# Optimization experiments

Hardware: AMD Instinct MI355X
Metric: run time of the kernel (lower is better)

## Reference

```python
import jax, jax.numpy as jnp
import numpy as np
from jax import lax

KERNEL_SIZE = 5
BOUNDARY_WIDTH = 10


def setup_inputs() -> dict:
    key = jax.random.key(0)
    x_in = jax.random.normal(key, (4, 16, 720, 1440), dtype=jnp.float32)
    return {"x_in": x_in}


def _box_sum(a, k):
    """Sum over a k x k window on the last two dims, zero-padded (SAME).
    Zero padding + mask-count division reproduces the clipped-window average."""
    window = (1,) * (a.ndim - 2) + (k, k)
    strides = (1,) * a.ndim
    return lax.reduce_window(a, jnp.array(0, a.dtype), lax.add, window, strides, "SAME")


def reference(x_in) -> jnp.ndarray:
    k = KERNEL_SIZE
    bw = BOUNDARY_WIDTH
    H, W = x_in.shape[-2], x_in.shape[-1]

    ii = jnp.arange(H)
    jj = jnp.arange(W)
    # boundary mask [H, W]: True within boundary_width of any edge
    mb = (((ii < bw) | (ii >= H - bw))[:, None]
          | ((jj < bw) | (jj >= W - bw))[None, :])
    mb_f = mb.astype(x_in.dtype)
    mi_f = 1.0 - mb_f

    # windowed sums of same-class neighbors (zero padding = clipped window)
    num_b = _box_sum(x_in * mb_f, k)   # contributions from boundary pixels
    num_i = _box_sum(x_in * mi_f, k)   # contributions from interior pixels
    cnt_b = _box_sum(mb_f, k)          # [H, W] counts, broadcast over leading dims
    cnt_i = _box_sum(mi_f, k)

    num = jnp.where(mb, num_b, num_i)
    cnt = jnp.where(mb, cnt_b, cnt_i)  # >= 1 wherever selected (pixel counts itself)
    return num / cnt
```

## Files before the change

### kernel.cpp

```cpp
#include <hip/hip_runtime.h>


#define HH 720
#define WW 1440
#define PLANE (HH * WW)
#define NPLANES 64


#define NG 354
#define NCHUNK 29
#define CHUNK 24

__device__ __forceinline__ float4 hsum5(const float* __restrict__ p) {
    const float2 l = *(const float2*)(p - 2);
    const float4 m = *(const float4*)(p);
    const float2 r = *(const float2*)(p + 4);
    float4 h;
    h.x = l.x + l.y + m.x + m.y + m.z;
    h.y = h.x - l.x + m.w;
    h.z = h.y - l.y + r.x;
    h.w = h.z - m.x + r.y;
    return h;
}

__global__ __launch_bounds__(256) void fast_kernel(const float* __restrict__ x,
                                                   float* __restrict__ out) {
    const int id = blockIdx.x * 256 + threadIdx.x;
    if (id >= NG * NCHUNK) return;
    const int chunk = id / NG;
    const int g     = id - chunk * NG;
    const int j0    = 12 + 4 * g;
    const int row0  = 12 + chunk * CHUNK;

    const float* __restrict__ xp = x + (size_t)blockIdx.y * PLANE;
    float* __restrict__ op       = out + (size_t)blockIdx.y * PLANE;

    float4 h[5];
#pragma unroll
    for (int t = 0; t < 4; ++t) {
        h[t] = hsum5(xp + (row0 - 2 + t) * WW + j0);
    }

#pragma unroll
    for (int t = 0; t < CHUNK; ++t) {
        const int r = row0 + t;
        h[(t + 4) % 5] = hsum5(xp + (r + 2) * WW + j0);
        float4 v;
        v.x = ((h[0].x + h[1].x) + (h[2].x + h[3].x)) + h[4].x;
        v.y = ((h[0].y + h[1].y) + (h[2].y + h[3].y)) + h[4].y;
        v.z = ((h[0].z + h[1].z) + (h[2].z + h[3].z)) + h[4].z;
        v.w = ((h[0].w + h[1].w) + (h[2].w + h[3].w)) + h[4].w;
        const float s = 1.0f / 25.0f;
        v.x *= s; v.y *= s; v.z *= s; v.w *= s;
        *(float4*)(op + r * WW + j0) = v;
    }
}


#define NEDGE 51264

__global__ __launch_bounds__(256) void edge_kernel(const float* __restrict__ x,
                                                   float* __restrict__ out) {
    const int p = blockIdx.x * 256 + threadIdx.x;
    if (p >= NEDGE) return;
    int i, j;
    if (p < 34560) {
        i = p / 1440;
        j = p - i * 1440;
        if (i >= 12) i += 696;
    } else {
        const int q  = p - 34560;
        const int qi = q / 24;
        const int r  = q - qi * 24;
        i = 12 + qi;
        j = (r < 12) ? r : r + 1416;
    }

    const float* __restrict__ xp = x + (size_t)blockIdx.y * PLANE;
    const bool cb = (i < 10) | (i >= 710) | (j < 10) | (j >= 1430);

    float s = 0.0f, cnt = 0.0f;
#pragma unroll
    for (int di = -2; di <= 2; ++di) {
#pragma unroll
        for (int dj = -2; dj <= 2; ++dj) {
            const int ni = i + di, nj = j + dj;
            const bool inb = ((unsigned)ni < (unsigned)HH) & ((unsigned)nj < (unsigned)WW);
            const bool nb  = (ni < 10) | (ni >= 710) | (nj < 10) | (nj >= 1430);
            const int ci = min(max(ni, 0), HH - 1);
            const int cj = min(max(nj, 0), WW - 1);
            const float v = xp[ci * WW + cj];
            const float w = (inb && (nb == cb)) ? 1.0f : 0.0f;
            s += w * v;
            cnt += w;
        }
    }
    out[(size_t)blockIdx.y * PLANE + i * WW + j] = s / cnt;
}

extern "C" void kernel_launch(void* const* d_in, const int* in_sizes, int n_in,
                              void* d_out, int out_size, void* d_ws, size_t ws_size,
                              hipStream_t stream) {
    const float* x = (const float*)d_in[0];
    float* out = (float*)d_out;

    dim3 gf((NG * NCHUNK + 255) / 256, NPLANES);
    hipLaunchKernelGGL(fast_kernel, gf, dim3(256), 0, stream, x, out);

    dim3 ge((NEDGE + 255) / 256, NPLANES);
    hipLaunchKernelGGL(edge_kernel, ge, dim3(256), 0, stream, x, out);
}
```

Before: 469.2 us.

## Fuse interior and edge kernels; widen to 8 columns with running vertical sum

Merges the interior fast kernel and the edge kernel into one launch, dispatching on blockIdx.x. Each interior thread now covers 8 columns instead of 4 and keeps a running vertical sum (add new row, subtract old) instead of re-adding all five row sums. Output writes use nontemporal stores. This removes a kernel launch and some redundant horizontal loads and adds, but raises register pressure per thread and halves the number of interior threads.

```diff
diff --git a/kernel.cpp b/kernel.cpp
--- a/kernel.cpp
+++ b/kernel.cpp
@@ -6,62 +6,77 @@
 #define PLANE (HH * WW)
 #define NPLANES 64
 
-
-#define NG 354
+#define NG8 177
 #define NCHUNK 29
 #define CHUNK 24
+#define NFAST (NG8 * NCHUNK)
+#define FAST_BLOCKS 21
 
-__device__ __forceinline__ float4 hsum5(const float* __restrict__ p) {
+#define NEDGE 51264
+#define EDGE_BLOCKS 201
+
+typedef float v4f __attribute__((ext_vector_type(4)));
+
+__device__ __forceinline__ void hsum8(const float* __restrict__ p, float h[8]) {
     const float2 l = *(const float2*)(p - 2);
-    const float4 m = *(const float4*)(p);
-    const float2 r = *(const float2*)(p + 4);
-    float4 h;
-    h.x = l.x + l.y + m.x + m.y + m.z;
-    h.y = h.x - l.x + m.w;
-    h.z = h.y - l.y + r.x;
-    h.w = h.z - m.x + r.y;
-    return h;
+    const float4 a = *(const float4*)(p);
+    const float4 b = *(const float4*)(p + 4);
+    const float2 r = *(const float2*)(p + 8);
+    h[0] = l.x + l.y + a.x + a.y + a.z;
+    h[1] = h[0] - l.x + a.w;
+    h[2] = h[1] - l.y + b.x;
+    h[3] = h[2] - a.x + b.y;
+    h[4] = h[3] - a.y + b.z;
+    h[5] = h[4] - a.z + b.w;
+    h[6] = h[5] - a.w + r.x;
+    h[7] = h[6] - b.x + r.y;
 }
 
-__global__ __launch_bounds__(256) void fast_kernel(const float* __restrict__ x,
-                                                   float* __restrict__ out) {
-    const int id = blockIdx.x * 256 + threadIdx.x;
-    if (id >= NG * NCHUNK) return;
-    const int chunk = id / NG;
-    const int g     = id - chunk * NG;
-    const int j0    = 12 + 4 * g;
-    const int row0  = 12 + chunk * CHUNK;
-
+__global__ __launch_bounds__(256) void smooth_kernel(const float* __restrict__ x,
+                                                     float* __restrict__ out) {
     const float* __restrict__ xp = x + (size_t)blockIdx.y * PLANE;
     float* __restrict__ op       = out + (size_t)blockIdx.y * PLANE;
 
-    float4 h[5];
+    if (blockIdx.x < FAST_BLOCKS) {
+        const int id = blockIdx.x * 256 + threadIdx.x;
+        if (id >= NFAST) return;
+        const int chunk = id / NG8;
+        const int g     = id - chunk * NG8;
+        const int j0    = 12 + 8 * g;
+        const int row0  = 12 + chunk * CHUNK;
+
+        float h[5][8];
+        float V[8];
+
 #pragma unroll
-    for (int t = 0; t < 4; ++t) {
-        h[t] = hsum5(xp + (row0 - 2 + t) * WW + j0);
+        for (int t = 0; t < 4; ++t) {
+            hsum8(xp + (row0 - 2 + t) * WW + j0, h[t]);
+        }
+#pragma unroll
+        for (int c = 0; c < 8; ++c) V[c] = h[0][c] + h[1][c] + h[2][c] + h[3][c];
+
+#pragma unroll
+        for (int t = 0; t < CHUNK; ++t) {
+            const int r = row0 + t;
+            float* hn = h[(t + 4) % 5];
+            const float* ho = h[t % 5];
+            hsum8(xp + (r + 2) * WW + j0, hn);
+
+            const float s = 1.0f / 25.0f;
+#pragma unroll
+            for (int c = 0; c < 8; ++c) V[c] += hn[c];
+            v4f v0, v1;
+            v0.x = V[0] * s; v0.y = V[1] * s; v0.z = V[2] * s; v0.w = V[3] * s;
+            v1.x = V[4] * s; v1.y = V[5] * s; v1.z = V[6] * s; v1.w = V[7] * s;
+            __builtin_nontemporal_store(v0, (v4f*)(op + r * WW + j0));
+            __builtin_nontemporal_store(v1, (v4f*)(op + r * WW + j0 + 4));
+#pragma unroll
+            for (int c = 0; c < 8; ++c) V[c] -= ho[c];
+        }
+        return;
     }
 
-#pragma unroll
-    for (int t = 0; t < CHUNK; ++t) {
-        const int r = row0 + t;
-        h[(t + 4) % 5] = hsum5(xp + (r + 2) * WW + j0);
-        float4 v;
-        v.x = ((h[0].x + h[1].x) + (h[2].x + h[3].x)) + h[4].x;
-        v.y = ((h[0].y + h[1].y) + (h[2].y + h[3].y)) + h[4].y;
-        v.z = ((h[0].z + h[1].z) + (h[2].z + h[3].z)) + h[4].z;
-        v.w = ((h[0].w + h[1].w) + (h[2].w + h[3].w)) + h[4].w;
-        const float s = 1.0f / 25.0f;
-        v.x *= s; v.y *= s; v.z *= s; v.w *= s;
-        *(float4*)(op + r * WW + j0) = v;
-    }
-}
-
-
-#define NEDGE 51264
-
-__global__ __launch_bounds__(256) void edge_kernel(const float* __restrict__ x,
-                                                   float* __restrict__ out) {
-    const int p = blockIdx.x * 256 + threadIdx.x;
+    const int p = (blockIdx.x - FAST_BLOCKS) * 256 + threadIdx.x;
     if (p >= NEDGE) return;
     int i, j;
     if (p < 34560) {
@@ -71,12 +86,11 @@
     } else {
         const int q  = p - 34560;
         const int qi = q / 24;
-        const int r  = q - qi * 24;
+        const int rr = q - qi * 24;
         i = 12 + qi;
-        j = (r < 12) ? r : r + 1416;
+        j = (rr < 12) ? rr : rr + 1416;
     }
 
-    const float* __restrict__ xp = x + (size_t)blockIdx.y * PLANE;
     const bool cb = (i < 10) | (i >= 710) | (j < 10) | (j >= 1430);
 
     float s = 0.0f, cnt = 0.0f;
@@ -95,7 +109,7 @@
             cnt += w;
         }
     }
-    out[(size_t)blockIdx.y * PLANE + i * WW + j] = s / cnt;
+    op[i * WW + j] = s / cnt;
 }
 
 extern "C" void kernel_launch(void* const* d_in, const int* in_sizes, int n_in,
@@ -104,9 +118,6 @@
     const float* x = (const float*)d_in[0];
     float* out = (float*)d_out;
 
-    dim3 gf((NG * NCHUNK + 255) / 256, NPLANES);
-    hipLaunchKernelGGL(fast_kernel, gf, dim3(256), 0, stream, x, out);
-
-    dim3 ge((NEDGE + 255) / 256, NPLANES);
-    hipLaunchKernelGGL(edge_kernel, ge, dim3(256), 0, stream, x, out);
+    dim3 grid(FAST_BLOCKS + EDGE_BLOCKS, NPLANES);
+    hipLaunchKernelGGL(smooth_kernel, grid, dim3(256), 0, stream, x, out);
 }
```

Result: slower. 529.4 us (+12.8%).
